# Kernel optimization log

Hardware: AMD Instinct MI355X
Metric: run time of the kernel (lower is better)

The kernel has to match this reference:

```python
import jax, jax.numpy as jnp
import numpy as np
from jax.scipy.special import logsumexp

SPARSITY = 0.0


def setup_inputs() -> dict:
    key = jax.random.key(0)
    k1, k2, k3, k4, k5 = jax.random.split(key, 5)
    N, M = 65536, 1024
    sample = jax.random.uniform(k1, (N, 2), dtype=jnp.float32)
    mu = jax.random.uniform(k2, (M, 2), dtype=jnp.float32)
    sigma_log = jax.random.uniform(k3, (M, 2), dtype=jnp.float32)
    theta = jax.random.normal(k4, (M,), dtype=jnp.float32)
    w = jax.random.normal(k5, (M, 1), dtype=jnp.float32)
    return {"sample": sample, "mu": mu, "sigma_log": sigma_log, "theta": theta, "w": w}


def reference(sample, mu, sigma_log, theta, w):
    # Anisotropic covariance entries: gamma_j = R(theta)^T diag(sig2) R(theta)
    sig2 = jnp.exp(-2.0 * sigma_log)            # [M,2], inverse variances
    a, b = sig2[:, 0], sig2[:, 1]
    c, s = jnp.cos(theta), jnp.sin(theta)
    g11 = a * c**2 + b * s**2                   # [M]
    g12 = (a - b) * c * s                       # [M]
    g22 = a * s**2 + b * c**2                   # [M]

    # Log weights: log_softmax(w) - sum(sigma_log) (normalization factor)
    wlog = jax.nn.log_softmax(w, axis=0)[:, 0] - sigma_log.sum(axis=1)  # [M]

    # All-pairs anisotropic quadratic form, fused per-coordinate (no [N,M,2] tensor)
    dx = sample[:, None, 0] - mu[None, :, 0]    # [N,M]
    dy = sample[:, None, 1] - mu[None, :, 1]    # [N,M]
    qf = g11 * dx * dx + 2.0 * g12 * dx * dy + g22 * dy * dy  # [N,M]

    # Log-density at each sample: logsumexp over mixture components
    ll = logsumexp(wlog[None, :] - qf, axis=1)  # [N]

    # Negative log-likelihood + sparsity penalty
    nll = -ll.sum() + SPARSITY * jnp.sqrt(jax.nn.softmax(w, axis=0)).sum()
    return nll
```

## Files before the change

kernel.cpp:

```cpp
#include <hip/hip_runtime.h>
#include <math.h>

#define LOG2E 1.4426950408889634f
#define LN2   0.6931471805599453f

typedef short bf8 __attribute__((ext_vector_type(8)));
typedef float f4  __attribute__((ext_vector_type(4)));

__device__ __forceinline__ unsigned short bf_hi(float x) {
    unsigned u = __float_as_uint(x);
    return (unsigned short)((u + 0x7FFFu + ((u >> 16) & 1u)) >> 16);
}

#define DPP_ADD(x, ctrl) \
    x += __int_as_float(__builtin_amdgcn_update_dpp(0, __float_as_int(x), ctrl, 0xF, 0xF, false))
__device__ __forceinline__ float row_sum16(float x) {
    DPP_ADD(x, 0x111);
    DPP_ADD(x, 0x112);
    DPP_ADD(x, 0x114);
    DPP_ADD(x, 0x118);
    return x;
}

__global__ __launch_bounds__(1024) void gm_mfma(
    const float* __restrict__ sample,
    const float* __restrict__ mu,
    const float* __restrict__ sigma_log,
    const float* __restrict__ theta,
    const float* __restrict__ w,
    float* __restrict__ out,
    int M)
{
    __shared__ __align__(16) unsigned short wrec[1024 * 40];
    __shared__ __align__(16) unsigned short srec[256 * 40];
    __shared__ float ws[16];
    __shared__ float psum[16 * 256];
    __shared__ float bsum[4];

    const int tid  = threadIdx.x;
    const int lane = tid & 63;
    const int wid  = tid >> 6;
    const int quad = lane >> 4;
    const int col  = lane & 15;

    const float wj = w[tid];
    float e = __expf(wj);
    #pragma unroll
    for (int off = 32; off > 0; off >>= 1)
        e += __shfl_down(e, off, 64);
    if (lane == 0) ws[wid] = e;
    __syncthreads();
    float tot = 0.0f;
    #pragma unroll
    for (int k = 0; k < 16; ++k) tot += ws[k];
    const float lse = __logf(tot);

    {
        const float sl0 = sigma_log[2 * tid + 0];
        const float sl1 = sigma_log[2 * tid + 1];
        const float a = __expf(-2.0f * sl0);
        const float b = __expf(-2.0f * sl1);
        const float th = theta[tid];
        const float c = __cosf(th);
        const float s = __sinf(th);

        const float g11 = a * c * c + b * s * s;
        const float g12 = (a - b) * c * s;
        const float g22 = a * s * s + b * c * c;

        const float mx = mu[2 * tid + 0];
        const float my = mu[2 * tid + 1];

        const float wlog = wj - lse - (sl0 + sl1);

        float cf[6];
        cf[0] = -g11 * LOG2E;
        cf[1] = -2.0f * g12 * LOG2E;
        cf[2] = -g22 * LOG2E;
        cf[3] = 2.0f * (g11 * mx + g12 * my) * LOG2E;
        cf[4] = 2.0f * (g12 * mx + g22 * my) * LOG2E;
        const float F = g11 * mx * mx + 2.0f * g12 * mx * my + g22 * my * my;
        cf[5] = (wlog - F) * LOG2E;

        unsigned short r[32];
        #pragma unroll
        for (int s2 = 0; s2 < 6; ++s2) {
            const unsigned short h = bf_hi(cf[s2]);
            const float hf = __uint_as_float((unsigned)h << 16);
            const unsigned short l = bf_hi(cf[s2] - hf);
            r[s2] = h; r[6 + s2] = l; r[12 + s2] = h;
        }
        #pragma unroll
        for (int s2 = 18; s2 < 32; ++s2) r[s2] = 0;
        unsigned* dst = (unsigned*)&wrec[tid * 40];
        #pragma unroll
        for (int k = 0; k < 16; ++k)
            dst[k] = ((unsigned)r[2 * k + 1] << 16) | r[2 * k];
    }

    if (tid < 256) {
        const float2 sv = ((const float2*)sample)[blockIdx.x * 256 + tid];
        float f[6];
        f[0] = sv.x * sv.x; f[1] = sv.x * sv.y; f[2] = sv.y * sv.y;
        f[3] = sv.x; f[4] = sv.y; f[5] = 1.0f;

        unsigned short r[32];
        #pragma unroll
        for (int s2 = 0; s2 < 6; ++s2) {
            const unsigned short h = bf_hi(f[s2]);
            const float hf = __uint_as_float((unsigned)h << 16);
            const unsigned short l = bf_hi(f[s2] - hf);
            r[s2] = h; r[6 + s2] = h; r[12 + s2] = l;
        }
        #pragma unroll
        for (int s2 = 18; s2 < 32; ++s2) r[s2] = 0;
        unsigned* dst = (unsigned*)&srec[tid * 40];
        #pragma unroll
        for (int k = 0; k < 16; ++k)
            dst[k] = ((unsigned)r[2 * k + 1] << 16) | r[2 * k];
    }
    __syncthreads();

    bf8 bfrag[4];
    #pragma unroll
    for (int ct = 0; ct < 4; ++ct) {
        const int comp = wid * 64 + ct * 16 + col;
        bfrag[ct] = *(const bf8*)&wrec[comp * 40 + quad * 8];
    }

    const f4 zero = {0.0f, 0.0f, 0.0f, 0.0f};
    for (int st = 0; st < 16; ++st) {
        const bf8 afrag = *(const bf8*)&srec[(st * 16 + col) * 40 + quad * 8];
        float a0 = 0.0f, a1 = 0.0f, a2 = 0.0f, a3 = 0.0f;
        #pragma unroll
        for (int ct = 0; ct < 4; ++ct) {
            const f4 d = __builtin_amdgcn_mfma_f32_16x16x32_bf16(
                afrag, bfrag[ct], zero, 0, 0, 0);
            a0 += __builtin_amdgcn_exp2f(d[0]);
            a1 += __builtin_amdgcn_exp2f(d[1]);
            a2 += __builtin_amdgcn_exp2f(d[2]);
            a3 += __builtin_amdgcn_exp2f(d[3]);
        }
        a0 = row_sum16(a0); a1 = row_sum16(a1);
        a2 = row_sum16(a2); a3 = row_sum16(a3);
        if (col == 15) {
            f4 o = {a0, a1, a2, a3};
            *(f4*)&psum[wid * 256 + st * 16 + quad * 4] = o;
        }
    }
    __syncthreads();

    if (tid < 256) {
        float t = 0.0f;
        #pragma unroll
        for (int k = 0; k < 16; ++k) t += psum[k * 256 + tid];
        float v = -LN2 * __builtin_amdgcn_logf(t);
        #pragma unroll
        for (int off = 32; off > 0; off >>= 1)
            v += __shfl_down(v, off, 64);
        if ((tid & 63) == 0) bsum[tid >> 6] = v;
    }
    __syncthreads();
    if (tid == 0)
        atomicAdd(out, (bsum[0] + bsum[1]) + (bsum[2] + bsum[3]));
}

extern "C" void kernel_launch(void* const* d_in, const int* in_sizes, int n_in,
                              void* d_out, int out_size, void* d_ws, size_t ws_size,
                              hipStream_t stream) {
    const float* sample    = (const float*)d_in[0];
    const float* mu        = (const float*)d_in[1];
    const float* sigma_log = (const float*)d_in[2];
    const float* theta     = (const float*)d_in[3];
    const float* w         = (const float*)d_in[4];
    float* out = (float*)d_out;

    const int M = in_sizes[3];
    const int N = in_sizes[0] / 2;

    hipMemsetAsync(out, 0, sizeof(float), stream);

    const int grid = N / 256;
    gm_mfma<<<grid, 1024, 0, stream>>>(sample, mu, sigma_log, theta, w, out, M);
}
```

Measured before the change: 77.07 us.

## Split mixture components across two blocks and combine with second reduction kernel

Each block now handles half of the mixture components for 256 samples, doubling the grid. Per-sample partial exp-sums go to a workspace buffer, and a second kernel adds the two halves, takes the log and reduces to the output. The aim is more blocks, better occupancy and smaller shared memory per block on the many-CU GPU. In exchange each block still pays the full softmax-normalisation prologue and sample setup, and there is an extra kernel launch plus a workspace round trip.

```diff
diff --git a/kernel.cpp b/kernel.cpp
--- a/kernel.cpp
+++ b/kernel.cpp
@@ -22,20 +22,19 @@
     return x;
 }
 
-__global__ __launch_bounds__(1024) void gm_mfma(
+__global__ __launch_bounds__(1024) void gm_pass1(
     const float* __restrict__ sample,
     const float* __restrict__ mu,
     const float* __restrict__ sigma_log,
     const float* __restrict__ theta,
     const float* __restrict__ w,
-    float* __restrict__ out,
-    int M)
+    float* __restrict__ part,
+    int N, int M)
 {
-    __shared__ __align__(16) unsigned short wrec[1024 * 40];
+    __shared__ __align__(16) unsigned short wrec[512 * 40];
     __shared__ __align__(16) unsigned short srec[256 * 40];
     __shared__ float ws[16];
     __shared__ float psum[16 * 256];
-    __shared__ float bsum[4];
 
     const int tid  = threadIdx.x;
     const int lane = tid & 63;
@@ -43,6 +42,11 @@
     const int quad = lane >> 4;
     const int col  = lane & 15;
 
+    const int half = blockIdx.x & 1;
+    const int sg   = blockIdx.x >> 1;
+    const int m0   = half * (M >> 1);
+    const int s0g  = sg * 256;
+
     const float wj = w[tid];
     float e = __expf(wj);
     #pragma unroll
@@ -55,12 +59,14 @@
     for (int k = 0; k < 16; ++k) tot += ws[k];
     const float lse = __logf(tot);
 
-    {
-        const float sl0 = sigma_log[2 * tid + 0];
-        const float sl1 = sigma_log[2 * tid + 1];
+    if (tid < 512) {
+        const int j = m0 + tid;
+        const float wjj = w[j];
+        const float sl0 = sigma_log[2 * j + 0];
+        const float sl1 = sigma_log[2 * j + 1];
         const float a = __expf(-2.0f * sl0);
         const float b = __expf(-2.0f * sl1);
-        const float th = theta[tid];
+        const float th = theta[j];
         const float c = __cosf(th);
         const float s = __sinf(th);
 
@@ -68,10 +74,10 @@
         const float g12 = (a - b) * c * s;
         const float g22 = a * s * s + b * c * c;
 
-        const float mx = mu[2 * tid + 0];
-        const float my = mu[2 * tid + 1];
-
-        const float wlog = wj - lse - (sl0 + sl1);
+        const float mx = mu[2 * j + 0];
+        const float my = mu[2 * j + 1];
+
+        const float wlog = wjj - lse - (sl0 + sl1);
 
         float cf[6];
         cf[0] = -g11 * LOG2E;
@@ -96,10 +102,9 @@
         #pragma unroll
         for (int k = 0; k < 16; ++k)
             dst[k] = ((unsigned)r[2 * k + 1] << 16) | r[2 * k];
-    }
-
-    if (tid < 256) {
-        const float2 sv = ((const float2*)sample)[blockIdx.x * 256 + tid];
+    } else if (tid < 768) {
+        const int si = tid - 512;
+        const float2 sv = ((const float2*)sample)[s0g + si];
         float f[6];
         f[0] = sv.x * sv.x; f[1] = sv.x * sv.y; f[2] = sv.y * sv.y;
         f[3] = sv.x; f[4] = sv.y; f[5] = 1.0f;
@@ -114,17 +119,17 @@
         }
         #pragma unroll
         for (int s2 = 18; s2 < 32; ++s2) r[s2] = 0;
-        unsigned* dst = (unsigned*)&srec[tid * 40];
+        unsigned* dst = (unsigned*)&srec[si * 40];
         #pragma unroll
         for (int k = 0; k < 16; ++k)
             dst[k] = ((unsigned)r[2 * k + 1] << 16) | r[2 * k];
     }
     __syncthreads();
 
-    bf8 bfrag[4];
-    #pragma unroll
-    for (int ct = 0; ct < 4; ++ct) {
-        const int comp = wid * 64 + ct * 16 + col;
+    bf8 bfrag[2];
+    #pragma unroll
+    for (int ct = 0; ct < 2; ++ct) {
+        const int comp = wid * 32 + ct * 16 + col;
         bfrag[ct] = *(const bf8*)&wrec[comp * 40 + quad * 8];
     }
 
@@ -133,7 +138,7 @@
         const bf8 afrag = *(const bf8*)&srec[(st * 16 + col) * 40 + quad * 8];
         float a0 = 0.0f, a1 = 0.0f, a2 = 0.0f, a3 = 0.0f;
         #pragma unroll
-        for (int ct = 0; ct < 4; ++ct) {
+        for (int ct = 0; ct < 2; ++ct) {
             const f4 d = __builtin_amdgcn_mfma_f32_16x16x32_bf16(
                 afrag, bfrag[ct], zero, 0, 0, 0);
             a0 += __builtin_amdgcn_exp2f(d[0]);
@@ -154,15 +159,34 @@
         float t = 0.0f;
         #pragma unroll
         for (int k = 0; k < 16; ++k) t += psum[k * 256 + tid];
-        float v = -LN2 * __builtin_amdgcn_logf(t);
-        #pragma unroll
-        for (int off = 32; off > 0; off >>= 1)
-            v += __shfl_down(v, off, 64);
-        if ((tid & 63) == 0) bsum[tid >> 6] = v;
-    }
-    __syncthreads();
-    if (tid == 0)
-        atomicAdd(out, (bsum[0] + bsum[1]) + (bsum[2] + bsum[3]));
+        part[half * N + s0g + tid] = t;
+    }
+}
+
+__global__ __launch_bounds__(1024) void gm_pass2(
+    const float* __restrict__ part,
+    float* __restrict__ out,
+    int N)
+{
+    const int i = blockIdx.x * 1024 + threadIdx.x;
+    const float t = part[i] + part[N + i];
+    float v = -LN2 * __builtin_amdgcn_logf(t);
+
+    #pragma unroll
+    for (int off = 32; off > 0; off >>= 1)
+        v += __shfl_down(v, off, 64);
+
+    __shared__ float bs[16];
+    const int lane = threadIdx.x & 63;
+    const int wid  = threadIdx.x >> 6;
+    if (lane == 0) bs[wid] = v;
+    __syncthreads();
+    if (threadIdx.x == 0) {
+        float t2 = 0.0f;
+        #pragma unroll
+        for (int k = 0; k < 16; ++k) t2 += bs[k];
+        atomicAdd(out, t2);
+    }
 }
 
 extern "C" void kernel_launch(void* const* d_in, const int* in_sizes, int n_in,
@@ -173,13 +197,18 @@
     const float* sigma_log = (const float*)d_in[2];
     const float* theta     = (const float*)d_in[3];
     const float* w         = (const float*)d_in[4];
-    float* out = (float*)d_out;
+    float* out  = (float*)d_out;
+    float* part = (float*)d_ws;
 
     const int M = in_sizes[3];
     const int N = in_sizes[0] / 2;
 
     hipMemsetAsync(out, 0, sizeof(float), stream);
 
-    const int grid = N / 256;
-    gm_mfma<<<grid, 1024, 0, stream>>>(sample, mu, sigma_log, theta, w, out, M);
-}
+    const int grid1 = (N / 256) * 2;
+    gm_pass1<<<grid1, 1024, 0, stream>>>(sample, mu, sigma_log, theta, w,
+                                         part, N, M);
+
+    const int grid2 = N / 1024;
+    gm_pass2<<<grid2, 1024, 0, stream>>>(part, out, N);
+}
```

New measurement: 83.74 us. 8.7% more time.

## Precompute component records once in a prep kernel and swap MFMA operand roles

Applied to the files above, without the earlier changes.

Moves the per-component coefficient computation (softmax normalisation, exp, sin/cos, bf16 hi/lo split) out of each of the 256 blocks into a single prep kernel that writes packed records to workspace. The main kernel then copies those records into LDS with vectorized loads. It also swaps the A/B operands of the MFMA so that each lane's four outputs belong to the same sample, letting the exp2 results be summed in-lane and reduced with two cross-lane shuffles instead of four DPP row reductions. This adds a second kernel launch and a global round-trip for the records, and replaces the memset with a write inside the prep kernel.

```diff
diff --git a/kernel.cpp b/kernel.cpp
--- a/kernel.cpp
+++ b/kernel.cpp
@@ -12,28 +12,80 @@
     return (unsigned short)((u + 0x7FFFu + ((u >> 16) & 1u)) >> 16);
 }
 
-#define DPP_ADD(x, ctrl) \
-    x += __int_as_float(__builtin_amdgcn_update_dpp(0, __float_as_int(x), ctrl, 0xF, 0xF, false))
-__device__ __forceinline__ float row_sum16(float x) {
-    DPP_ADD(x, 0x111);
-    DPP_ADD(x, 0x112);
-    DPP_ADD(x, 0x114);
-    DPP_ADD(x, 0x118);
-    return x;
-}
-
-__global__ __launch_bounds__(1024) void gm_mfma(
-    const float* __restrict__ sample,
+__global__ __launch_bounds__(1024) void gm_prep(
     const float* __restrict__ mu,
     const float* __restrict__ sigma_log,
     const float* __restrict__ theta,
     const float* __restrict__ w,
-    float* __restrict__ out,
-    int M)
+    unsigned* __restrict__ grec,
+    float* __restrict__ out)
+{
+    const int j = threadIdx.x;
+    const int lane = j & 63;
+    const int wid  = j >> 6;
+
+    const float wj = w[j];
+    float e = __expf(wj);
+    #pragma unroll
+    for (int off = 32; off > 0; off >>= 1)
+        e += __shfl_down(e, off, 64);
+    __shared__ float ws[16];
+    if (lane == 0) ws[wid] = e;
+    __syncthreads();
+    float tot = 0.0f;
+    #pragma unroll
+    for (int k = 0; k < 16; ++k) tot += ws[k];
+    const float lse = __logf(tot);
+
+    const float sl0 = sigma_log[2 * j + 0];
+    const float sl1 = sigma_log[2 * j + 1];
+    const float a = __expf(-2.0f * sl0);
+    const float b = __expf(-2.0f * sl1);
+    const float th = theta[j];
+    const float c = __cosf(th);
+    const float s = __sinf(th);
+
+    const float g11 = a * c * c + b * s * s;
+    const float g12 = (a - b) * c * s;
+    const float g22 = a * s * s + b * c * c;
+    const float mx = mu[2 * j + 0];
+    const float my = mu[2 * j + 1];
+    const float wlog = wj - lse - (sl0 + sl1);
+
+    float cf[6];
+    cf[0] = -g11 * LOG2E;
+    cf[1] = -2.0f * g12 * LOG2E;
+    cf[2] = -g22 * LOG2E;
+    cf[3] = 2.0f * (g11 * mx + g12 * my) * LOG2E;
+    cf[4] = 2.0f * (g12 * mx + g22 * my) * LOG2E;
+    const float F = g11 * mx * mx + 2.0f * g12 * mx * my + g22 * my * my;
+    cf[5] = (wlog - F) * LOG2E;
+
+    unsigned short r[32];
+    #pragma unroll
+    for (int q = 0; q < 6; ++q) {
+        const unsigned short h = bf_hi(cf[q]);
+        const float hf = __uint_as_float((unsigned)h << 16);
+        const unsigned short l = bf_hi(cf[q] - hf);
+        r[q] = h; r[6 + q] = l; r[12 + q] = h;
+    }
+    #pragma unroll
+    for (int q = 18; q < 32; ++q) r[q] = 0;
+    unsigned* dst = grec + j * 20;
+    #pragma unroll
+    for (int k = 0; k < 16; ++k)
+        dst[k] = ((unsigned)r[2 * k + 1] << 16) | r[2 * k];
+
+    if (j == 0) out[0] = 0.0f;
+}
+
+__global__ __launch_bounds__(1024) void gm_main(
+    const float* __restrict__ sample,
+    const float4* __restrict__ grec4,
+    float* __restrict__ out)
 {
     __shared__ __align__(16) unsigned short wrec[1024 * 40];
     __shared__ __align__(16) unsigned short srec[256 * 40];
-    __shared__ float ws[16];
     __shared__ float psum[16 * 256];
     __shared__ float bsum[4];
 
@@ -43,77 +95,26 @@
     const int quad = lane >> 4;
     const int col  = lane & 15;
 
-    const float wj = w[tid];
-    float e = __expf(wj);
+    float4* wl = (float4*)wrec;
     #pragma unroll
-    for (int off = 32; off > 0; off >>= 1)
-        e += __shfl_down(e, off, 64);
-    if (lane == 0) ws[wid] = e;
-    __syncthreads();
-    float tot = 0.0f;
-    #pragma unroll
-    for (int k = 0; k < 16; ++k) tot += ws[k];
-    const float lse = __logf(tot);
-
-    {
-        const float sl0 = sigma_log[2 * tid + 0];
-        const float sl1 = sigma_log[2 * tid + 1];
-        const float a = __expf(-2.0f * sl0);
-        const float b = __expf(-2.0f * sl1);
-        const float th = theta[tid];
-        const float c = __cosf(th);
-        const float s = __sinf(th);
-
-        const float g11 = a * c * c + b * s * s;
-        const float g12 = (a - b) * c * s;
-        const float g22 = a * s * s + b * c * c;
-
-        const float mx = mu[2 * tid + 0];
-        const float my = mu[2 * tid + 1];
-
-        const float wlog = wj - lse - (sl0 + sl1);
-
-        float cf[6];
-        cf[0] = -g11 * LOG2E;
-        cf[1] = -2.0f * g12 * LOG2E;
-        cf[2] = -g22 * LOG2E;
-        cf[3] = 2.0f * (g11 * mx + g12 * my) * LOG2E;
-        cf[4] = 2.0f * (g12 * mx + g22 * my) * LOG2E;
-        const float F = g11 * mx * mx + 2.0f * g12 * mx * my + g22 * my * my;
-        cf[5] = (wlog - F) * LOG2E;
-
-        unsigned short r[32];
-        #pragma unroll
-        for (int s2 = 0; s2 < 6; ++s2) {
-            const unsigned short h = bf_hi(cf[s2]);
-            const float hf = __uint_as_float((unsigned)h << 16);
-            const unsigned short l = bf_hi(cf[s2] - hf);
-            r[s2] = h; r[6 + s2] = l; r[12 + s2] = h;
-        }
-        #pragma unroll
-        for (int s2 = 18; s2 < 32; ++s2) r[s2] = 0;
-        unsigned* dst = (unsigned*)&wrec[tid * 40];
-        #pragma unroll
-        for (int k = 0; k < 16; ++k)
-            dst[k] = ((unsigned)r[2 * k + 1] << 16) | r[2 * k];
-    }
+    for (int i = 0; i < 5; ++i)
+        wl[i * 1024 + tid] = grec4[i * 1024 + tid];
 
     if (tid < 256) {
         const float2 sv = ((const float2*)sample)[blockIdx.x * 256 + tid];
         float f[6];
         f[0] = sv.x * sv.x; f[1] = sv.x * sv.y; f[2] = sv.y * sv.y;
         f[3] = sv.x; f[4] = sv.y; f[5] = 1.0f;
-
         unsigned short r[32];
         #pragma unroll
-        for (int s2 = 0; s2 < 6; ++s2) {
-            const unsigned short h = bf_hi(f[s2]);
+        for (int q = 0; q < 6; ++q) {
+            const unsigned short h = bf_hi(f[q]);
             const float hf = __uint_as_float((unsigned)h << 16);
-            const unsigned short l = bf_hi(f[s2] - hf);
-            r[s2] = h; r[6 + s2] = h; r[12 + s2] = l;
+            const unsigned short l = bf_hi(f[q] - hf);
+            r[q] = h; r[6 + q] = h; r[12 + q] = l;
         }
         #pragma unroll
-        for (int s2 = 18; s2 < 32; ++s2) r[s2] = 0;
+        for (int q = 18; q < 32; ++q) r[q] = 0;
         unsigned* dst = (unsigned*)&srec[tid * 40];
         #pragma unroll
         for (int k = 0; k < 16; ++k)
@@ -121,32 +122,25 @@
     }
     __syncthreads();
 
-    bf8 bfrag[4];
+    bf8 afrag[4];
     #pragma unroll
-    for (int ct = 0; ct < 4; ++ct) {
-        const int comp = wid * 64 + ct * 16 + col;
-        bfrag[ct] = *(const bf8*)&wrec[comp * 40 + quad * 8];
-    }
+    for (int ct = 0; ct < 4; ++ct)
+        afrag[ct] = *(const bf8*)&wrec[(wid * 64 + ct * 16 + col) * 40 + quad * 8];
 
     const f4 zero = {0.0f, 0.0f, 0.0f, 0.0f};
     for (int st = 0; st < 16; ++st) {
-        const bf8 afrag = *(const bf8*)&srec[(st * 16 + col) * 40 + quad * 8];
-        float a0 = 0.0f, a1 = 0.0f, a2 = 0.0f, a3 = 0.0f;
+        const bf8 bfrag = *(const bf8*)&srec[(st * 16 + col) * 40 + quad * 8];
+        float acc = 0.0f;
         #pragma unroll
         for (int ct = 0; ct < 4; ++ct) {
             const f4 d = __builtin_amdgcn_mfma_f32_16x16x32_bf16(
-                afrag, bfrag[ct], zero, 0, 0, 0);
-            a0 += __builtin_amdgcn_exp2f(d[0]);
-            a1 += __builtin_amdgcn_exp2f(d[1]);
-            a2 += __builtin_amdgcn_exp2f(d[2]);
-            a3 += __builtin_amdgcn_exp2f(d[3]);
+                afrag[ct], bfrag, zero, 0, 0, 0);
+            acc += (__builtin_amdgcn_exp2f(d[0]) + __builtin_amdgcn_exp2f(d[1]))
+                 + (__builtin_amdgcn_exp2f(d[2]) + __builtin_amdgcn_exp2f(d[3]));
         }
-        a0 = row_sum16(a0); a1 = row_sum16(a1);
-        a2 = row_sum16(a2); a3 = row_sum16(a3);
-        if (col == 15) {
-            f4 o = {a0, a1, a2, a3};
-            *(f4*)&psum[wid * 256 + st * 16 + quad * 4] = o;
-        }
+        acc += __shfl_xor(acc, 16, 64);
+        acc += __shfl_xor(acc, 32, 64);
+        if (quad == 0) psum[wid * 256 + st * 16 + col] = acc;
     }
     __syncthreads();
 
@@ -174,12 +168,12 @@
     const float* theta     = (const float*)d_in[3];
     const float* w         = (const float*)d_in[4];
     float* out = (float*)d_out;
+    unsigned* grec = (unsigned*)d_ws;
 
-    const int M = in_sizes[3];
     const int N = in_sizes[0] / 2;
 
-    hipMemsetAsync(out, 0, sizeof(float), stream);
+    gm_prep<<<1, 1024, 0, stream>>>(mu, sigma_log, theta, w, grec, out);
 
     const int grid = N / 256;
-    gm_mfma<<<grid, 1024, 0, stream>>>(sample, mu, sigma_log, theta, w, out, M);
+    gm_main<<<grid, 1024, 0, stream>>>(sample, (const float4*)grec, out);
 }
```

After: 77.36 us. Within noise of the previous version (+0.4%).
